# Kernel tuning notes

Hardware: AMD Instinct MI355X
Metric: run time of the kernel (lower is better)

## Reference

```python
import jax, jax.numpy as jnp
import numpy as np

# Module hyperparameters (from init_kwargs)
LATENT = 1024
H = 16          # num query heads
HK = 4          # num key/value heads (GQA)
D = 64          # head_dim
CAUSAL = True
QKV_OUT = (3 * H + 2 * HK) * D  # 3584, as defined in the source module


def setup_inputs() -> dict:
    key = jax.random.key(0)
    k1, k2, k3 = jax.random.split(key, 3)
    B, S = 2, 2048
    x = jax.random.normal(k1, (B, S, LATENT), dtype=jnp.float32)
    # nn.Linear weights are [out_features, in_features]; scale like torch default init
    w_qkv = jax.random.normal(k2, (QKV_OUT, LATENT), dtype=jnp.float32) / np.sqrt(LATENT)
    w_out = jax.random.normal(k3, (LATENT, H * D), dtype=jnp.float32) / np.sqrt(H * D)
    return {"x": x, "w_qkv": w_qkv, "w_out": w_out}


def reference(x, w_qkv, w_out):
    B, S, _ = x.shape
    scale = 1.0 / np.sqrt(D).astype(np.float32)

    # Fused QKV projection: [B,S,(3H+2HK)*D]
    qkv = jnp.einsum('bsl,ol->bso', x, w_qkv)

    # Split: q takes H heads, k and v take HK heads each (GQA).
    # (The extra 2*H*D columns of the fused projection are allocated by the
    #  source module but unused by q/k/v, matching its layer sizing.)
    q = qkv[..., : H * D].reshape(B, S, H, D)
    k = qkv[..., H * D:(H + HK) * D].reshape(B, S, HK, D)
    v = qkv[..., (H + HK) * D:(H + 2 * HK) * D].reshape(B, S, HK, D)

    # Expand KV heads to match query heads (group factor H // HK)
    rep = H // HK
    k = jnp.repeat(k, rep, axis=2)  # [B,S,H,D]
    v = jnp.repeat(v, rep, axis=2)

    # Scaled dot-product attention
    scores = jnp.einsum('bshd,bthd->bhst', q, k) * scale  # [B,H,S,S]
    if CAUSAL:
        causal_mask = jnp.tril(jnp.ones((S, S), dtype=bool))
        scores = jnp.where(causal_mask, scores, jnp.finfo(scores.dtype).min)
    attn = jax.nn.softmax(scores, axis=-1)
    out = jnp.einsum('bhst,bthd->bshd', attn, v).reshape(B, S, H * D)

    # Output projection back to latent_size
    return jnp.einsum('bso,lo->bsl', out, w_out)
```

## Files before the change

kernel.cpp:

```cpp
#include <hip/hip_runtime.h>
#include <hip/hip_bf16.h>
#include <math.h>

typedef __attribute__((ext_vector_type(8))) short bf16x8;
typedef __attribute__((ext_vector_type(4))) float f32x4;
typedef __attribute__((ext_vector_type(16))) float f32x16;
typedef unsigned short u16;
typedef unsigned int   u32;

#define DEVINL __device__ __forceinline__

DEVINL u16 f2bf(float x) {
    u32 u = __float_as_uint(x);
    u += 0x7fffu + ((u >> 16) & 1u);
    return (u16)(u >> 16);
}

DEVINL void gl_lds16(const void* g, void* s) {
    __builtin_amdgcn_global_load_lds(
        (const __attribute__((address_space(1))) u32*)g,
        (__attribute__((address_space(3))) u32*)s,
        16, 0, 0);
}

DEVINL f32x4 mfma16(bf16x8 a, bf16x8 b, f32x4 c) {
    return __builtin_amdgcn_mfma_f32_16x16x32_bf16(a, b, c, 0, 0, 0);
}
DEVINL f32x16 mfma32(bf16x8 a, bf16x8 b, f32x16 c) {
    return __builtin_amdgcn_mfma_f32_32x32x16_bf16(a, b, c, 0, 0, 0);
}

__global__ void cvt3(const float* __restrict__ x, const float* __restrict__ wq,
                     const float* __restrict__ wo,
                     u16* __restrict__ xb, u16* __restrict__ wqb, u16* __restrict__ wob) {
    int i = blockIdx.x * 256 + threadIdx.x;
    const float* s; u16* d; int j;
    if (i < 1048576)      { s = x;  d = xb;  j = i; }
    else if (i < 1441792) { s = wq; d = wqb; j = i - 1048576; }
    else                  { s = wo; d = wob; j = i - 1441792; }
    float4 v = ((const float4*)s)[j];
    ushort4 o;
    o.x = f2bf(v.x); o.y = f2bf(v.y); o.z = f2bf(v.z); o.w = f2bf(v.w);
    ((ushort4*)d)[j] = o;
}

template<int EP>
__launch_bounds__(128)
__global__ void gemm_w2(const u16* __restrict__ A, const u16* __restrict__ B,
                        const int N, const int K,
                        float* __restrict__ Cf,
                        u16* __restrict__ Qo, u16* __restrict__ Ko, u16* __restrict__ Vo)
{
    __shared__ __align__(16) u16 As[64 * 64];
    __shared__ __align__(16) u16 Bs[128 * 64];
    const int tid  = threadIdx.x;
    const int lane = tid & 63;
    const int w    = tid >> 6;
    const int l31  = lane & 31;
    const int half = lane >> 5;
    const int lr   = lane >> 3;
    const int lc   = lane & 7;
    const int swst = lc ^ lr;
    const int rk   = lane & 7;
    const int m0 = blockIdx.y * 64;
    const int n0 = blockIdx.x * 128;

    f32x16 acc[2][2];
    for (int mf = 0; mf < 2; mf++)
        for (int nf = 0; nf < 2; nf++)
            for (int i = 0; i < 16; i++) acc[mf][nf][i] = 0.f;

    const u16* Ap = A + (m0 + w * 32 + lr) * K + swst * 8;
    const u16* Bp = B + (n0 + w * 64 + lr) * K + swst * 8;

    for (int k0 = 0; k0 < K; k0 += 64) {
        for (int j = 0; j < 4; j++)
            gl_lds16(Ap + j * 8 * K + k0, As + (w * 32 + j * 8) * 64);
        for (int j = 0; j < 8; j++)
            gl_lds16(Bp + j * 8 * K + k0, Bs + (w * 64 + j * 8) * 64);
        __syncthreads();
        bf16x8 af[2][4], bfv[2][4];
        for (int ks = 0; ks < 4; ks++) {
            const int ch = ((ks * 2 + half) ^ rk) * 8;
            for (int mf = 0; mf < 2; mf++)
                af[mf][ks] = *(const bf16x8*)&As[(mf * 32 + l31) * 64 + ch];
            for (int nf = 0; nf < 2; nf++)
                bfv[nf][ks] = *(const bf16x8*)&Bs[(w * 64 + nf * 32 + l31) * 64 + ch];
        }
        for (int ks = 0; ks < 4; ks++)
            for (int mf = 0; mf < 2; mf++)
                for (int nf = 0; nf < 2; nf++)
                    acc[mf][nf] = mfma32(af[mf][ks], bfv[nf][ks], acc[mf][nf]);
        __syncthreads();
    }

    if (EP == 0) {
        for (int mf = 0; mf < 2; mf++)
            for (int nf = 0; nf < 2; nf++)
                for (int r = 0; r < 16; r++) {
                    int row = m0 + mf * 32 + (r & 3) + 8 * (r >> 2) + 4 * half;
                    int col = n0 + w * 64 + nf * 32 + l31;
                    Cf[row * N + col] = acc[mf][nf][r];
                }
    } else {
        const float qsc = 0.18033688011112042f;
        for (int mf = 0; mf < 2; mf++)
            for (int nf = 0; nf < 2; nf++)
                for (int r = 0; r < 16; r++) {
                    int row = m0 + mf * 32 + (r & 3) + 8 * (r >> 2) + 4 * half;
                    int col = n0 + w * 64 + nf * 32 + l31;
                    int bb = row >> 11, ss = row & 2047;
                    if (col < 1024) {
                        int hh = col >> 6, dd = col & 63;
                        Qo[((bb * 16 + hh) * 2048 + ss) * 64 + dd] = f2bf(acc[mf][nf][r] * qsc);
                    } else if (col < 1280) {
                        int c = col - 1024, hh = c >> 6, dd = c & 63;
                        Ko[((bb * 4 + hh) * 2048 + ss) * 64 + dd] = f2bf(acc[mf][nf][r]);
                    } else {
                        int c = col - 1280, hh = c >> 6, dd = c & 63;
                        Vo[((bb * 4 + hh) * 64 + dd) * 2048 + ss] = f2bf(acc[mf][nf][r]);
                    }
                }
    }
}

__launch_bounds__(256)
__global__ void attn_kernel(const u16* __restrict__ Qg, const u16* __restrict__ Kg,
                            const u16* __restrict__ Vtg, u16* __restrict__ Og)
{
    __shared__ __align__(16) u16 Ks[2][64 * 64];
    __shared__ __align__(16) u16 Vs[2][64 * 64];
    __shared__ __align__(16) u16 Ps[64 * 64];

    const int tid  = threadIdx.x;
    const int lane = tid & 63;
    const int w    = tid >> 6;
    const int quad = lane >> 4;
    const int lcol = lane & 15;
    const int lr   = lane >> 3;
    const int lc   = lane & 7;
    const int swst = lc ^ lr;
    const int rk   = lcol & 7;

    const int p  = blockIdx.x;
    const int h  = blockIdx.y;
    const int b  = blockIdx.z;
    const int hk = h >> 2;

    const u16* Qp = Qg  + (b * 16 + h) * 2048 * 64;
    const u16* Kp = Kg  + (b * 4 + hk) * 2048 * 64;
    const u16* Vp = Vtg + (b * 4 + hk) * 64 * 2048;

    for (int pass = 0; pass < 2; pass++) {
        const int qi = pass ? (31 - p) : p;
        const int q0 = qi * 64;
        const int nt = qi + 1;

        bf16x8 aqr[2];
        for (int ks = 0; ks < 2; ks++)
            aqr[ks] = *(const bf16x8*)(Qp + (q0 + w * 16 + lcol) * 64 + ks * 32 + quad * 8);

        for (int j = 0; j < 2; j++) {
            const int r = w * 16 + j * 8 + lr;
            gl_lds16(Kp + r * 64 + swst * 8,   &Ks[0][w * 1024 + j * 512]);
            gl_lds16(Vp + r * 2048 + swst * 8, &Vs[0][w * 1024 + j * 512]);
        }

        f32x4 o[4];
        float l_p[4];
        for (int db = 0; db < 4; db++)
            for (int i = 0; i < 4; i++) o[db][i] = 0.f;
        for (int i = 0; i < 4; i++) l_p[i] = 0.f;

        __syncthreads();

        for (int ti = 0; ti < nt; ti++) {
            const int cur = ti & 1;
            if (ti + 1 < nt) {
                const int nb = cur ^ 1;
                const int t0n = (ti + 1) * 64;
                for (int j = 0; j < 2; j++) {
                    const int r = w * 16 + j * 8 + lr;
                    gl_lds16(Kp + (t0n + r) * 64 + swst * 8, &Ks[nb][w * 1024 + j * 512]);
                    gl_lds16(Vp + r * 2048 + t0n + swst * 8, &Vs[nb][w * 1024 + j * 512]);
                }
            }

            f32x4 s[4];
            for (int cb = 0; cb < 4; cb++)
                for (int i = 0; i < 4; i++) s[cb][i] = 0.f;
            for (int ks = 0; ks < 2; ks++) {
                const int chq = ((ks * 4 + quad) ^ rk) * 8;
                for (int cb = 0; cb < 4; cb++) {
                    bf16x8 bk = *(const bf16x8*)&Ks[cur][(cb * 16 + lcol) * 64 + chq];
                    s[cb] = mfma16(aqr[ks], bk, s[cb]);
                }
            }

            if (ti == nt - 1) {
                for (int cb = 0; cb < 4; cb++)
                    for (int i = 0; i < 4; i++) {
                        const bool masked = (cb * 16 + lcol) > (w * 16 + quad * 4 + i);
                        s[cb][i] = masked ? -INFINITY : s[cb][i];
                    }
            }

            for (int cb = 0; cb < 4; cb++)
                for (int i = 0; i < 4; i++) {
                    const float pv = exp2f(s[cb][i]);
                    s[cb][i] = pv;
                    l_p[i] += pv;
                }

            for (int cb = 0; cb < 4; cb++)
                for (int i = 0; i < 4; i++) {
                    const int rl = quad * 4 + i;
                    const int cc = cb * 2 + (lcol >> 3);
                    Ps[(w * 16 + rl) * 64 + ((cc ^ (rl & 7)) << 3) + lc] =
                        (u16)(__float_as_uint(s[cb][i]) >> 16);
                }

            for (int kt = 0; kt < 2; kt++) {
                const int chp = ((kt * 4 + quad) ^ rk) * 8;
                bf16x8 ap = *(const bf16x8*)&Ps[(w * 16 + lcol) * 64 + chp];
                for (int db = 0; db < 4; db++) {
                    bf16x8 bv = *(const bf16x8*)&Vs[cur][(db * 16 + lcol) * 64 + chp];
                    o[db] = mfma16(ap, bv, o[db]);
                }
            }
            __syncthreads();
        }

        for (int i = 0; i < 4; i++) {
            float l = l_p[i];
            for (int x = 1; x < 16; x <<= 1) l += __shfl_xor(l, x);
            const float inv = 1.0f / l;
            const int srow = q0 + w * 16 + quad * 4 + i;
            for (int db = 0; db < 4; db++)
                Og[(b * 2048 + srow) * 1024 + h * 64 + db * 16 + lcol] = f2bf(o[db][i] * inv);
        }
    }
}

extern "C" void kernel_launch(void* const* d_in, const int* in_sizes, int n_in,
                              void* d_out, int out_size, void* d_ws, size_t ws_size,
                              hipStream_t stream) {
    const float* x     = (const float*)d_in[0];
    const float* w_qkv = (const float*)d_in[1];
    const float* w_out = (const float*)d_in[2];
    float* out = (float*)d_out;
    char* ws = (char*)d_ws;

    u16* xb  = (u16*)(ws);
    u16* wqb = (u16*)(ws + 8  * 1024 * 1024);
    u16* wob = (u16*)(ws + 11 * 1024 * 1024);
    u16* qb  = (u16*)(ws + 13 * 1024 * 1024);
    u16* kb  = (u16*)(ws + 21 * 1024 * 1024);
    u16* vtb = (u16*)(ws + 23 * 1024 * 1024);
    u16* aob = (u16*)(ws);

    cvt3<<<6656, 256, 0, stream>>>(x, w_qkv, w_out, xb, wqb, wob);

    gemm_w2<1><<<dim3(12, 64), 128, 0, stream>>>(xb, wqb, 1536, 1024,
                                                 nullptr, qb, kb, vtb);
    attn_kernel<<<dim3(16, 16, 2), 256, 0, stream>>>(qb, kb, vtb, aob);
    gemm_w2<0><<<dim3(8, 64), 128, 0, stream>>>(aob, wob, 1024, 1024,
                                                out, nullptr, nullptr, nullptr);
}
```

Baseline: 175.6 us.

## Use 32x32 MFMA with 128-row query tiles in attention kernel

```diff
diff --git a/kernel.cpp b/kernel.cpp
--- a/kernel.cpp
+++ b/kernel.cpp
@@ -23,9 +23,6 @@
         16, 0, 0);
 }
 
-DEVINL f32x4 mfma16(bf16x8 a, bf16x8 b, f32x4 c) {
-    return __builtin_amdgcn_mfma_f32_16x16x32_bf16(a, b, c, 0, 0, 0);
-}
 DEVINL f32x16 mfma32(bf16x8 a, bf16x8 b, f32x16 c) {
     return __builtin_amdgcn_mfma_f32_32x32x16_bf16(a, b, c, 0, 0, 0);
 }
@@ -130,115 +127,118 @@
 {
     __shared__ __align__(16) u16 Ks[2][64 * 64];
     __shared__ __align__(16) u16 Vs[2][64 * 64];
-    __shared__ __align__(16) u16 Ps[64 * 64];
+    __shared__ __align__(16) u16 Ps[128 * 64];
 
     const int tid  = threadIdx.x;
     const int lane = tid & 63;
     const int w    = tid >> 6;
-    const int quad = lane >> 4;
-    const int lcol = lane & 15;
+    const int l31  = lane & 31;
+    const int half = lane >> 5;
     const int lr   = lane >> 3;
     const int lc   = lane & 7;
     const int swst = lc ^ lr;
-    const int rk   = lcol & 7;
-
-    const int p  = blockIdx.x;
-    const int h  = blockIdx.y;
-    const int b  = blockIdx.z;
-    const int hk = h >> 2;
+    const int rk7  = l31 & 7;
+
+    const int x   = blockIdx.x;
+    const int qi0 = x & 15;
+    const int rest = x >> 4;
+    const int h   = rest & 15;
+    const int b   = rest >> 4;
+    const int qi  = b ? (15 - qi0) : qi0;
+    const int hk  = h >> 2;
+    const int q0  = qi * 128;
+    const int nt  = 2 * qi + 2;
 
     const u16* Qp = Qg  + (b * 16 + h) * 2048 * 64;
     const u16* Kp = Kg  + (b * 4 + hk) * 2048 * 64;
     const u16* Vp = Vtg + (b * 4 + hk) * 64 * 2048;
 
-    for (int pass = 0; pass < 2; pass++) {
-        const int qi = pass ? (31 - p) : p;
-        const int q0 = qi * 64;
-        const int nt = qi + 1;
-
-        bf16x8 aqr[2];
-        for (int ks = 0; ks < 2; ks++)
-            aqr[ks] = *(const bf16x8*)(Qp + (q0 + w * 16 + lcol) * 64 + ks * 32 + quad * 8);
-
-        for (int j = 0; j < 2; j++) {
-            const int r = w * 16 + j * 8 + lr;
-            gl_lds16(Kp + r * 64 + swst * 8,   &Ks[0][w * 1024 + j * 512]);
-            gl_lds16(Vp + r * 2048 + swst * 8, &Vs[0][w * 1024 + j * 512]);
+    bf16x8 aqr[4];
+    for (int ks = 0; ks < 4; ks++)
+        aqr[ks] = *(const bf16x8*)(Qp + (q0 + w * 32 + l31) * 64 + ks * 16 + half * 8);
+
+    for (int j = 0; j < 2; j++) {
+        const int r = w * 16 + j * 8 + lr;
+        gl_lds16(Kp + r * 64 + swst * 8,   &Ks[0][(w * 16 + j * 8) * 64]);
+        gl_lds16(Vp + r * 2048 + swst * 8, &Vs[0][(w * 16 + j * 8) * 64]);
+    }
+
+    f32x16 o[2];
+    float l_p[16];
+    for (int nf = 0; nf < 2; nf++)
+        for (int i = 0; i < 16; i++) o[nf][i] = 0.f;
+    for (int r = 0; r < 16; r++) l_p[r] = 0.f;
+
+    __syncthreads();
+
+    for (int ti = 0; ti < nt; ti++) {
+        const int cur = ti & 1;
+        const int t0  = ti * 64;
+        if (ti + 1 < nt) {
+            const int nb = cur ^ 1;
+            const int t0n = (ti + 1) * 64;
+            for (int j = 0; j < 2; j++) {
+                const int r = w * 16 + j * 8 + lr;
+                gl_lds16(Kp + (t0n + r) * 64 + swst * 8, &Ks[nb][(w * 16 + j * 8) * 64]);
+                gl_lds16(Vp + r * 2048 + t0n + swst * 8, &Vs[nb][(w * 16 + j * 8) * 64]);
+            }
         }
 
-        f32x4 o[4];
-        float l_p[4];
-        for (int db = 0; db < 4; db++)
-            for (int i = 0; i < 4; i++) o[db][i] = 0.f;
-        for (int i = 0; i < 4; i++) l_p[i] = 0.f;
-
+        if (t0 <= q0 + w * 32 + 31) {
+            f32x16 s[2];
+            for (int nf = 0; nf < 2; nf++)
+                for (int i = 0; i < 16; i++) s[nf][i] = 0.f;
+            for (int ks = 0; ks < 4; ks++) {
+                const int ch = ((2 * ks + half) ^ rk7) * 8;
+                for (int nf = 0; nf < 2; nf++) {
+                    bf16x8 bk = *(const bf16x8*)&Ks[cur][(nf * 32 + l31) * 64 + ch];
+                    s[nf] = mfma32(aqr[ks], bk, s[nf]);
+                }
+            }
+
+            if (t0 + 63 > q0 + w * 32) {
+                for (int nf = 0; nf < 2; nf++)
+                    for (int r = 0; r < 16; r++) {
+                        const int rl = (r & 3) + 8 * (r >> 2) + 4 * half;
+                        const int rg = q0 + w * 32 + rl;
+                        const int cg = t0 + nf * 32 + l31;
+                        if (cg > rg) s[nf][r] = -INFINITY;
+                    }
+            }
+
+            for (int r = 0; r < 16; r++) {
+                const int rl = (r & 3) + 8 * (r >> 2) + 4 * half;
+                for (int nf = 0; nf < 2; nf++) {
+                    const float pv = exp2f(s[nf][r]);
+                    l_p[r] += pv;
+                    const int cc = nf * 4 + (l31 >> 3);
+                    Ps[(w * 32 + rl) * 64 + ((cc ^ (rl & 7)) << 3) + (l31 & 7)] =
+                        (u16)(__float_as_uint(pv) >> 16);
+                }
+            }
+
+            bf16x8 ap[4];
+            for (int ks = 0; ks < 4; ks++)
+                ap[ks] = *(const bf16x8*)&Ps[(w * 32 + l31) * 64 + (((2 * ks + half) ^ rk7) << 3)];
+            for (int ks = 0; ks < 4; ks++) {
+                const int ch = ((2 * ks + half) ^ rk7) * 8;
+                for (int nf = 0; nf < 2; nf++) {
+                    bf16x8 bv = *(const bf16x8*)&Vs[cur][(nf * 32 + l31) * 64 + ch];
+                    o[nf] = mfma32(ap[ks], bv, o[nf]);
+                }
+            }
+        }
         __syncthreads();
-
-        for (int ti = 0; ti < nt; ti++) {
-            const int cur = ti & 1;
-            if (ti + 1 < nt) {
-                const int nb = cur ^ 1;
-                const int t0n = (ti + 1) * 64;
-                for (int j = 0; j < 2; j++) {
-                    const int r = w * 16 + j * 8 + lr;
-                    gl_lds16(Kp + (t0n + r) * 64 + swst * 8, &Ks[nb][w * 1024 + j * 512]);
-                    gl_lds16(Vp + r * 2048 + t0n + swst * 8, &Vs[nb][w * 1024 + j * 512]);
-                }
-            }
-
-            f32x4 s[4];
-            for (int cb = 0; cb < 4; cb++)
-                for (int i = 0; i < 4; i++) s[cb][i] = 0.f;
-            for (int ks = 0; ks < 2; ks++) {
-                const int chq = ((ks * 4 + quad) ^ rk) * 8;
-                for (int cb = 0; cb < 4; cb++) {
-                    bf16x8 bk = *(const bf16x8*)&Ks[cur][(cb * 16 + lcol) * 64 + chq];
-                    s[cb] = mfma16(aqr[ks], bk, s[cb]);
-                }
-            }
-
-            if (ti == nt - 1) {
-                for (int cb = 0; cb < 4; cb++)
-                    for (int i = 0; i < 4; i++) {
-                        const bool masked = (cb * 16 + lcol) > (w * 16 + quad * 4 + i);
-                        s[cb][i] = masked ? -INFINITY : s[cb][i];
-                    }
-            }
-
-            for (int cb = 0; cb < 4; cb++)
-                for (int i = 0; i < 4; i++) {
-                    const float pv = exp2f(s[cb][i]);
-                    s[cb][i] = pv;
-                    l_p[i] += pv;
-                }
-
-            for (int cb = 0; cb < 4; cb++)
-                for (int i = 0; i < 4; i++) {
-                    const int rl = quad * 4 + i;
-                    const int cc = cb * 2 + (lcol >> 3);
-                    Ps[(w * 16 + rl) * 64 + ((cc ^ (rl & 7)) << 3) + lc] =
-                        (u16)(__float_as_uint(s[cb][i]) >> 16);
-                }
-
-            for (int kt = 0; kt < 2; kt++) {
-                const int chp = ((kt * 4 + quad) ^ rk) * 8;
-                bf16x8 ap = *(const bf16x8*)&Ps[(w * 16 + lcol) * 64 + chp];
-                for (int db = 0; db < 4; db++) {
-                    bf16x8 bv = *(const bf16x8*)&Vs[cur][(db * 16 + lcol) * 64 + chp];
-                    o[db] = mfma16(ap, bv, o[db]);
-                }
-            }
-            __syncthreads();
-        }
-
-        for (int i = 0; i < 4; i++) {
-            float l = l_p[i];
-            for (int x = 1; x < 16; x <<= 1) l += __shfl_xor(l, x);
-            const float inv = 1.0f / l;
-            const int srow = q0 + w * 16 + quad * 4 + i;
-            for (int db = 0; db < 4; db++)
-                Og[(b * 2048 + srow) * 1024 + h * 64 + db * 16 + lcol] = f2bf(o[db][i] * inv);
-        }
+    }
+
+    for (int r = 0; r < 16; r++) {
+        float l = l_p[r];
+        for (int xm = 1; xm < 32; xm <<= 1) l += __shfl_xor(l, xm);
+        const float inv = 1.0f / l;
+        const int rl = (r & 3) + 8 * (r >> 2) + 4 * half;
+        const int row = q0 + w * 32 + rl;
+        for (int nf = 0; nf < 2; nf++)
+            Og[(b * 2048 + row) * 1024 + h * 64 + nf * 32 + l31] = f2bf(o[nf][r] * inv);
     }
 }
 
@@ -263,7 +263,7 @@
 
     gemm_w2<1><<<dim3(12, 64), 128, 0, stream>>>(xb, wqb, 1536, 1024,
                                                  nullptr, qb, kb, vtb);
-    attn_kernel<<<dim3(16, 16, 2), 256, 0, stream>>>(qb, kb, vtb, aob);
+    attn_kernel<<<dim3(512), 256, 0, stream>>>(qb, kb, vtb, aob);
     gemm_w2<0><<<dim3(8, 64), 128, 0, stream>>>(aob, wob, 1024, 1024,
                                                 out, nullptr, nullptr, nullptr);
 }
```

Result: slower. 190.9 us (+8.7%).
